# Performance work log

Hardware: AMD Instinct MI355X
Metric: run time of the kernel (lower is better)

## Reference

```python
import jax, jax.numpy as jnp
import numpy as np

D_MODEL = 1024
D_HIDDEN = 4096
NUM_BANKS = 16
NUM_SELECTED = 2


def setup_inputs() -> dict:
    key = jax.random.key(0)
    ks = jax.random.split(key, 7)
    s = 0.02
    return {
        "tensor": jax.random.normal(ks[0], (4, 1024, D_MODEL), dtype=jnp.float32),
        "Wr": jax.random.normal(ks[1], (D_MODEL, NUM_BANKS), dtype=jnp.float32) * s,
        "br": jnp.zeros((NUM_BANKS,), dtype=jnp.float32),
        "W1": jax.random.normal(ks[2], (NUM_BANKS, D_MODEL, D_HIDDEN), dtype=jnp.float32) * s,
        "b1": jnp.zeros((NUM_BANKS, D_HIDDEN), dtype=jnp.float32),
        "W2": jax.random.normal(ks[3], (NUM_BANKS, D_HIDDEN, D_MODEL), dtype=jnp.float32) * s,
        "b2": jnp.zeros((NUM_BANKS, D_MODEL), dtype=jnp.float32),
    }


def reference(tensor, Wr, br, W1, b1, W2, b2):
    # Router: softmax over banks, keep top-k probabilities (BankSelector)
    logits = jnp.einsum("bsd,de->bse", tensor, Wr) + br          # [B,S,E]
    probs = jax.nn.softmax(logits, axis=-1)
    topv, topi = jax.lax.top_k(probs, NUM_SELECTED)              # [B,S,K]
    # Dense gate [B,S,E]: selected banks carry their router probability,
    # all other banks are zeroed (equivalent to sparse dispatch/combine).
    gate = jnp.sum(jax.nn.one_hot(topi, NUM_BANKS, dtype=tensor.dtype)
                   * topv[..., None], axis=-2)                    # [B,S,E]
    # Banked expert FFN (BankedLinear x2 with ReLU between)
    h = jax.nn.relu(jnp.einsum("bsd,edh->bseh", tensor, W1) + b1)  # [B,S,E,Dh]
    y = jnp.einsum("bseh,ehm->bsem", h, W2) + b2                   # [B,S,E,Dm]
    # Weighted combine across selected banks
    out = jnp.einsum("bse,bsem->bsm", gate, y)                     # [B,S,Dm]
    return out
```

## Files before the change

kernel.cpp:

```cpp
#include <hip/hip_runtime.h>
#include <stdint.h>

#define D_MODEL   1024
#define D_HIDDEN  4096
#define NBANKS    16
#define NTOK      4096

#define BM 128
#define BN 128
#define BK 32
#define TBUF (BM * BK)
#define KS2 4

typedef __attribute__((ext_vector_type(8))) short bf16x8;
typedef __attribute__((ext_vector_type(4))) float f32x4;
typedef __attribute__((ext_vector_type(4))) unsigned int u32x4;
typedef __attribute__((ext_vector_type(2))) unsigned int u32x2;

__device__ __forceinline__ unsigned short f2bf(float f) {
  unsigned u = __builtin_bit_cast(unsigned, f);
  u += 0x7FFFu + ((u >> 16) & 1u);
  return (unsigned short)(u >> 16);
}

__device__ __forceinline__ unsigned cvtpk(float lo, float hi) {
  unsigned r;
  asm("v_cvt_pk_bf16_f32 %0, %1, %2" : "=v"(r) : "v"(lo), "v"(hi));
  return r;
}

__device__ __forceinline__ int sidx(int r, int k) {
  return (r << 5) + ((((k >> 3) ^ ((r >> 2) & 3)) << 3) | (k & 7));
}

__global__ __launch_bounds__(256) void zero_out_k(float4* __restrict__ out4,
                                                  int* __restrict__ counts) {
  size_t i = (size_t)blockIdx.x * 256 + threadIdx.x;
  out4[i] = make_float4(0.f, 0.f, 0.f, 0.f);
  if (blockIdx.x == 0 && threadIdx.x < NBANKS) counts[threadIdx.x] = 0;
}

__global__ __launch_bounds__(256) void cvtx_k(const float* __restrict__ X,
                                              unsigned short* __restrict__ Xb) {
  const size_t i = ((size_t)blockIdx.x * 256 + threadIdx.x) * 8;
  const float4 a = *(const float4*)(X + i);
  const float4 b = *(const float4*)(X + i + 4);
  u32x4 v;
  v[0] = cvtpk(a.x, a.y); v[1] = cvtpk(a.z, a.w);
  v[2] = cvtpk(b.x, b.y); v[3] = cvtpk(b.z, b.w);
  *(u32x4*)(Xb + i) = v;
}

__global__ __launch_bounds__(64) void router_k(const float* __restrict__ x,
                                               const float* __restrict__ Wr,
                                               const float* __restrict__ br,
                                               int* __restrict__ topIdx,
                                               float* __restrict__ topGate) {
  const int t = blockIdx.x;
  const int l = threadIdx.x;
  const float* xr = x + (size_t)t * D_MODEL;

  float acc[NBANKS];
#pragma unroll
  for (int e = 0; e < NBANKS; ++e) acc[e] = 0.f;

  for (int d = l; d < D_MODEL; d += 64) {
    const float xv = xr[d];
    const float* wrow = Wr + (size_t)d * NBANKS;
#pragma unroll
    for (int e = 0; e < NBANKS; ++e) acc[e] += xv * wrow[e];
  }
#pragma unroll
  for (int e = 0; e < NBANKS; ++e) {
#pragma unroll
    for (int m = 1; m < 64; m <<= 1) acc[e] += __shfl_xor(acc[e], m, 64);
  }
#pragma unroll
  for (int e = 0; e < NBANKS; ++e) acc[e] += br[e];

  if (l == 0) {
    float mx = acc[0];
#pragma unroll
    for (int e = 1; e < NBANKS; ++e) mx = fmaxf(mx, acc[e]);
    float p[NBANKS];
    float s = 0.f;
#pragma unroll
    for (int e = 0; e < NBANKS; ++e) { p[e] = expf(acc[e] - mx); s += p[e]; }
    int i0 = 0; float v0 = p[0];
#pragma unroll
    for (int e = 1; e < NBANKS; ++e) if (p[e] > v0) { v0 = p[e]; i0 = e; }
    int i1 = -1; float v1 = -1.f;
#pragma unroll
    for (int e = 0; e < NBANKS; ++e) if (e != i0 && p[e] > v1) { v1 = p[e]; i1 = e; }
    const float inv = 1.f / s;
    topIdx[2 * t]     = i0;
    topIdx[2 * t + 1] = i1;
    topGate[2 * t]     = v0 * inv;
    topGate[2 * t + 1] = v1 * inv;
  }
}

__global__ __launch_bounds__(256) void build_lists_k(const int* __restrict__ topIdx,
                                                     const float* __restrict__ topGate,
                                                     int* __restrict__ counts,
                                                     int* __restrict__ rowlist,
                                                     float* __restrict__ gatelist) {
  const int t = blockIdx.x * 256 + threadIdx.x;
  if (t >= NTOK) return;
#pragma unroll
  for (int k = 0; k < 2; ++k) {
    const int e = topIdx[2 * t + k];
    const int p = atomicAdd(&counts[e], 1);
    rowlist[e * NTOK + p]  = t;
    gatelist[e * NTOK + p] = topGate[2 * t + k];
  }
}

__global__ void scan_k(const int* __restrict__ counts, int* __restrict__ bankOff) {
  if (threadIdx.x == 0) {
    int s = 0;
#pragma unroll
    for (int e = 0; e < NBANKS; ++e) { bankOff[e] = s; s += counts[e]; }
    bankOff[NBANKS] = s;
  }
}

__global__ __launch_bounds__(256, 2) void gemm1_k(const unsigned short* __restrict__ Xb,
                                                  const float* __restrict__ W1,
                                                  const float* __restrict__ b1,
                                                  const int* __restrict__ counts,
                                                  const int* __restrict__ bankOff,
                                                  const int* __restrict__ rowlist,
                                                  unsigned short* __restrict__ H) {
  const int e   = blockIdx.z;
  const int cnt = counts[e];
  const int m0  = blockIdx.y * BM;
  if (m0 >= cnt) return;
  const int n0  = blockIdx.x * BN;

  const int tid  = threadIdx.x;
  const int lane = tid & 63;
  const int w    = tid >> 6;
  const int wm   = (w >> 1) * 64;
  const int wn   = (w & 1) * 64;

  __shared__ unsigned short Xs[2 * TBUF];
  __shared__ unsigned short Ws[2 * TBUF];

  const int arow = tid >> 1;
  const int ak   = (tid & 1) * 16;
  const int gi   = min(m0 + arow, cnt - 1);
  const int tok  = rowlist[e * NTOK + gi];
  const unsigned short* Asrc = Xb + (size_t)tok * D_MODEL + ak;
  const int xo0 = sidx(arow, ak);
  const int xo1 = sidx(arow, ak + 8);

  const int n4 = 4 * (tid & 31);
  const int k4 = 4 * (tid >> 5);
  const float* Bsrc = W1 + (size_t)e * D_MODEL * D_HIDDEN + (size_t)k4 * D_HIDDEN + n0 + n4;
  int wo[4];
#pragma unroll
  for (int i = 0; i < 4; ++i) wo[i] = sidx(n4 + i, k4);

  const int fr = lane & 15;
  const int fc = (lane >> 4) * 8;
  int aoff[4], boff[4];
#pragma unroll
  for (int i = 0; i < 4; ++i) {
    aoff[i] = sidx(wm + i * 16 + fr, fc);
    boff[i] = sidx(wn + i * 16 + fr, fc);
  }

  bf16x8 ra0, ra1;
  float rbf[4][4];

  f32x4 acc[4][4];
#pragma unroll
  for (int i = 0; i < 4; ++i)
#pragma unroll
    for (int j = 0; j < 4; ++j)
#pragma unroll
      for (int r = 0; r < 4; ++r) acc[i][j][r] = 0.f;

  unsigned short* xc = &Xs[0];       unsigned short* wc = &Ws[0];
  unsigned short* xn = &Xs[TBUF];    unsigned short* wn_ = &Ws[TBUF];

  auto LOAD = [&](int t) {
    const unsigned short* ap = Asrc + t * BK;
    ra0 = *(const bf16x8*)(ap);
    ra1 = *(const bf16x8*)(ap + 8);
    const float* bp = Bsrc + (size_t)t * BK * D_HIDDEN;
#pragma unroll
    for (int kk = 0; kk < 4; ++kk)
      *(float4*)&rbf[kk][0] = *(const float4*)(bp + (size_t)kk * D_HIDDEN);
  };

  auto WRITE = [&](unsigned short* xs, unsigned short* ws) {
    *(bf16x8*)(xs + xo0) = ra0;
    *(bf16x8*)(xs + xo1) = ra1;
#pragma unroll
    for (int i = 0; i < 4; ++i) {
      u32x2 v;
      v[0] = cvtpk(rbf[0][i], rbf[1][i]);
      v[1] = cvtpk(rbf[2][i], rbf[3][i]);
      *(u32x2*)(ws + wo[i]) = v;
    }
  };

  auto COMPUTE = [&](const unsigned short* xs, const unsigned short* ws) {
    bf16x8 af[4], bb[4];
#pragma unroll
    for (int mb = 0; mb < 4; ++mb) af[mb] = *(const bf16x8*)(xs + aoff[mb]);
#pragma unroll
    for (int nb = 0; nb < 4; ++nb) bb[nb] = *(const bf16x8*)(ws + boff[nb]);
#pragma unroll
    for (int mb = 0; mb < 4; ++mb)
#pragma unroll
      for (int nb = 0; nb < 4; ++nb)
        acc[mb][nb] = __builtin_amdgcn_mfma_f32_16x16x32_bf16(af[mb], bb[nb], acc[mb][nb], 0, 0, 0);
  };

  const int NT = D_MODEL / BK;
  LOAD(0);
  WRITE(xc, wc);
  __syncthreads();
#pragma unroll 1
  for (int t = 0; t < NT; ++t) {
    if (t + 1 < NT) LOAD(t + 1);
    __builtin_amdgcn_sched_barrier(0);
    COMPUTE(xc, wc);
    if (t + 1 < NT) WRITE(xn, wn_);
    __syncthreads();
    unsigned short* t0 = xc; xc = xn;  xn  = t0;
    unsigned short* t1 = wc; wc = wn_; wn_ = t1;
  }

  const int hb = bankOff[e] + m0;
  const int rq = (lane >> 4) * 4;
#pragma unroll
  for (int nb = 0; nb < 4; ++nb) {
    const int col = n0 + wn + nb * 16 + fr;
    const float bias = b1[e * D_HIDDEN + col];
#pragma unroll
    for (int mb = 0; mb < 4; ++mb)
#pragma unroll
      for (int r = 0; r < 4; ++r) {
        const int rowT = wm + mb * 16 + rq + r;
        if (m0 + rowT < cnt) {
          float v = acc[mb][nb][r] + bias;
          v = fmaxf(v, 0.f);
          H[(size_t)(hb + rowT) * D_HIDDEN + col] = f2bf(v);
        }
      }
  }
}

__global__ __launch_bounds__(256, 2) void gemm2_k(const unsigned short* __restrict__ H,
                                                  const float* __restrict__ W2,
                                                  const float* __restrict__ b2,
                                                  const int* __restrict__ counts,
                                                  const int* __restrict__ bankOff,
                                                  const int* __restrict__ rowlist,
                                                  const float* __restrict__ gatelist,
                                                  float* __restrict__ out) {
  const int z   = blockIdx.z;
  const int e   = z >> 2;
  const int kc  = z & 3;
  const int cnt = counts[e];
  const int m0  = blockIdx.y * BM;
  if (m0 >= cnt) return;
  const int n0  = blockIdx.x * BN;
  const int kc0 = kc * (D_HIDDEN / KS2);

  const int tid  = threadIdx.x;
  const int lane = tid & 63;
  const int w    = tid >> 6;
  const int wm   = (w >> 1) * 64;
  const int wn   = (w & 1) * 64;

  __shared__ unsigned short Xs[2 * TBUF];
  __shared__ unsigned short Ws[2 * TBUF];

  const int arow = tid >> 1;
  const int ak   = (tid & 1) * 16;
  const int hb   = bankOff[e];
  const int gi   = hb + min(m0 + arow, cnt - 1);
  const unsigned short* Asrc = H + (size_t)gi * D_HIDDEN + kc0 + ak;
  const int xo0 = sidx(arow, ak);
  const int xo1 = sidx(arow, ak + 8);

  const int n4 = 4 * (tid & 31);
  const int k4 = 4 * (tid >> 5);
  const float* Bsrc = W2 + (size_t)e * D_HIDDEN * D_MODEL + (size_t)(kc0 + k4) * D_MODEL + n0 + n4;
  int wo[4];
#pragma unroll
  for (int i = 0; i < 4; ++i) wo[i] = sidx(n4 + i, k4);

  const int fr = lane & 15;
  const int fc = (lane >> 4) * 8;
  int aoff[4], boff[4];
#pragma unroll
  for (int i = 0; i < 4; ++i) {
    aoff[i] = sidx(wm + i * 16 + fr, fc);
    boff[i] = sidx(wn + i * 16 + fr, fc);
  }

  bf16x8 ra0, ra1;
  float rbf[4][4];

  f32x4 acc[4][4];
#pragma unroll
  for (int i = 0; i < 4; ++i)
#pragma unroll
    for (int j = 0; j < 4; ++j)
#pragma unroll
      for (int r = 0; r < 4; ++r) acc[i][j][r] = 0.f;

  unsigned short* xc = &Xs[0];       unsigned short* wc = &Ws[0];
  unsigned short* xn = &Xs[TBUF];    unsigned short* wn_ = &Ws[TBUF];

  auto LOAD = [&](int t) {
    const unsigned short* ap = Asrc + t * BK;
    ra0 = *(const bf16x8*)(ap);
    ra1 = *(const bf16x8*)(ap + 8);
    const float* bp = Bsrc + (size_t)t * BK * D_MODEL;
#pragma unroll
    for (int kk = 0; kk < 4; ++kk)
      *(float4*)&rbf[kk][0] = *(const float4*)(bp + (size_t)kk * D_MODEL);
  };

  auto WRITE = [&](unsigned short* xs, unsigned short* ws) {
    *(bf16x8*)(xs + xo0) = ra0;
    *(bf16x8*)(xs + xo1) = ra1;
#pragma unroll
    for (int i = 0; i < 4; ++i) {
      u32x2 v;
      v[0] = cvtpk(rbf[0][i], rbf[1][i]);
      v[1] = cvtpk(rbf[2][i], rbf[3][i]);
      *(u32x2*)(ws + wo[i]) = v;
    }
  };

  auto COMPUTE = [&](const unsigned short* xs, const unsigned short* ws) {
    bf16x8 af[4], bb[4];
#pragma unroll
    for (int mb = 0; mb < 4; ++mb) af[mb] = *(const bf16x8*)(xs + aoff[mb]);
#pragma unroll
    for (int nb = 0; nb < 4; ++nb) bb[nb] = *(const bf16x8*)(ws + boff[nb]);
#pragma unroll
    for (int mb = 0; mb < 4; ++mb)
#pragma unroll
      for (int nb = 0; nb < 4; ++nb)
        acc[mb][nb] = __builtin_amdgcn_mfma_f32_16x16x32_bf16(af[mb], bb[nb], acc[mb][nb], 0, 0, 0);
  };

  const int NT = (D_HIDDEN / KS2) / BK;
  LOAD(0);
  WRITE(xc, wc);
  __syncthreads();
#pragma unroll 1
  for (int t = 0; t < NT; ++t) {
    if (t + 1 < NT) LOAD(t + 1);
    __builtin_amdgcn_sched_barrier(0);
    COMPUTE(xc, wc);
    if (t + 1 < NT) WRITE(xn, wn_);
    __syncthreads();
    unsigned short* t0 = xc; xc = xn;  xn  = t0;
    unsigned short* t1 = wc; wc = wn_; wn_ = t1;
  }

  const int rq = (lane >> 4) * 4;
  float bias[4];
#pragma unroll
  for (int nb = 0; nb < 4; ++nb)
    bias[nb] = (kc == 0) ? b2[e * D_MODEL + n0 + wn + nb * 16 + fr] : 0.f;

#pragma unroll
  for (int mb = 0; mb < 4; ++mb)
#pragma unroll
    for (int r = 0; r < 4; ++r) {
      const int rowT = wm + mb * 16 + rq + r;
      if (m0 + rowT < cnt) {
        const int si = e * NTOK + m0 + rowT;
        const int tok = rowlist[si];
        const float g = gatelist[si];
        float* orow = out + (size_t)tok * D_MODEL;
#pragma unroll
        for (int nb = 0; nb < 4; ++nb) {
          const int col = n0 + wn + nb * 16 + fr;
          atomicAdd(&orow[col], g * (acc[mb][nb][r] + bias[nb]));
        }
      }
    }
}

extern "C" void kernel_launch(void* const* d_in, const int* in_sizes, int n_in,
                              void* d_out, int out_size, void* d_ws, size_t ws_size,
                              hipStream_t stream) {
  const float* X  = (const float*)d_in[0];
  const float* Wr = (const float*)d_in[1];
  const float* br = (const float*)d_in[2];
  const float* W1 = (const float*)d_in[3];
  const float* b1 = (const float*)d_in[4];
  const float* W2 = (const float*)d_in[5];
  const float* b2 = (const float*)d_in[6];
  float* out = (float*)d_out;

  char* w = (char*)d_ws;
  int*   topIdx   = (int*)(w);
  float* topGate  = (float*)(w + (32 << 10));
  int*   counts   = (int*)(w + (64 << 10));
  int*   bankOff  = (int*)(w + (64 << 10) + 256);
  int*   rowlist  = (int*)(w + (66 << 10));
  float* gatelist = (float*)(w + (66 << 10) + NBANKS * NTOK * 4);
  unsigned short* Xb = (unsigned short*)(w + (1 << 20));
  unsigned short* H  = (unsigned short*)(w + (16 << 20));

  const size_t needed = (size_t)(16 << 20) + (size_t)(NTOK * 2) * D_HIDDEN * 2;
  if (ws_size < needed) return;

  zero_out_k<<<dim3(4096), dim3(256), 0, stream>>>((float4*)out, counts);
  cvtx_k<<<dim3(NTOK * D_MODEL / 8 / 256), dim3(256), 0, stream>>>(X, Xb);
  router_k<<<dim3(NTOK), dim3(64), 0, stream>>>(X, Wr, br, topIdx, topGate);
  build_lists_k<<<dim3(16), dim3(256), 0, stream>>>(topIdx, topGate, counts, rowlist, gatelist);
  scan_k<<<dim3(1), dim3(64), 0, stream>>>(counts, bankOff);
  gemm1_k<<<dim3(D_HIDDEN / BN, NTOK / BM, NBANKS), dim3(256), 0, stream>>>(
      Xb, W1, b1, counts, bankOff, rowlist, H);
  gemm2_k<<<dim3(D_MODEL / BN, NTOK / BM, NBANKS * KS2), dim3(256), 0, stream>>>(
      H, W2, b2, counts, bankOff, rowlist, gatelist, out);
}
```

Measured before the change: 450.1 us.

## Compact grouped-GEMM grid via precomputed tile list and adjust LDS swizzle

```diff
diff --git a/kernel.cpp b/kernel.cpp
--- a/kernel.cpp
+++ b/kernel.cpp
@@ -11,6 +11,7 @@
 #define BK 32
 #define TBUF (BM * BK)
 #define KS2 4
+#define MAXT 512
 
 typedef __attribute__((ext_vector_type(8))) short bf16x8;
 typedef __attribute__((ext_vector_type(4))) float f32x4;
@@ -30,7 +31,7 @@
 }
 
 __device__ __forceinline__ int sidx(int r, int k) {
-  return (r << 5) + ((((k >> 3) ^ ((r >> 2) & 3)) << 3) | (k & 7));
+  return (r << 5) + ((((k >> 3) ^ ((r >> 1) & 3)) << 3) | (k & 7));
 }
 
 __global__ __launch_bounds__(256) void zero_out_k(float4* __restrict__ out4,
@@ -116,12 +117,24 @@
   }
 }
 
-__global__ void scan_k(const int* __restrict__ counts, int* __restrict__ bankOff) {
+__global__ void scan_k(const int* __restrict__ counts, int* __restrict__ bankOff,
+                       int* __restrict__ tileE, int* __restrict__ tileM,
+                       int* __restrict__ nT) {
   if (threadIdx.x == 0) {
     int s = 0;
-#pragma unroll
-    for (int e = 0; e < NBANKS; ++e) { bankOff[e] = s; s += counts[e]; }
+    int t = 0;
+    for (int e = 0; e < NBANKS; ++e) {
+      bankOff[e] = s;
+      const int c = counts[e];
+      s += c;
+      for (int m = 0; m < c; m += BM) {
+        tileE[t] = e;
+        tileM[t] = m;
+        ++t;
+      }
+    }
     bankOff[NBANKS] = s;
+    nT[0] = t;
   }
 }
 
@@ -131,11 +144,15 @@
                                                   const int* __restrict__ counts,
                                                   const int* __restrict__ bankOff,
                                                   const int* __restrict__ rowlist,
+                                                  const int* __restrict__ tileE,
+                                                  const int* __restrict__ tileM,
+                                                  const int* __restrict__ nT,
                                                   unsigned short* __restrict__ H) {
-  const int e   = blockIdx.z;
+  const int tI = blockIdx.y;
+  if (tI >= nT[0]) return;
+  const int e   = tileE[tI];
+  const int m0  = tileM[tI];
   const int cnt = counts[e];
-  const int m0  = blockIdx.y * BM;
-  if (m0 >= cnt) return;
   const int n0  = blockIdx.x * BN;
 
   const int tid  = threadIdx.x;
@@ -262,13 +279,16 @@
                                                   const int* __restrict__ bankOff,
                                                   const int* __restrict__ rowlist,
                                                   const float* __restrict__ gatelist,
+                                                  const int* __restrict__ tileE,
+                                                  const int* __restrict__ tileM,
+                                                  const int* __restrict__ nT,
                                                   float* __restrict__ out) {
-  const int z   = blockIdx.z;
-  const int e   = z >> 2;
-  const int kc  = z & 3;
+  const int tI = blockIdx.y >> 2;
+  const int kc = blockIdx.y & 3;
+  if (tI >= nT[0]) return;
+  const int e   = tileE[tI];
+  const int m0  = tileM[tI];
   const int cnt = counts[e];
-  const int m0  = blockIdx.y * BM;
-  if (m0 >= cnt) return;
   const int n0  = blockIdx.x * BN;
   const int kc0 = kc * (D_HIDDEN / KS2);
 
@@ -413,6 +433,9 @@
   int*   bankOff  = (int*)(w + (64 << 10) + 256);
   int*   rowlist  = (int*)(w + (66 << 10));
   float* gatelist = (float*)(w + (66 << 10) + NBANKS * NTOK * 4);
+  int*   tileE    = (int*)(w + (600 << 10));
+  int*   tileM    = (int*)(w + (604 << 10));
+  int*   nT       = (int*)(w + (608 << 10));
   unsigned short* Xb = (unsigned short*)(w + (1 << 20));
   unsigned short* H  = (unsigned short*)(w + (16 << 20));
 
@@ -423,9 +446,9 @@
   cvtx_k<<<dim3(NTOK * D_MODEL / 8 / 256), dim3(256), 0, stream>>>(X, Xb);
   router_k<<<dim3(NTOK), dim3(64), 0, stream>>>(X, Wr, br, topIdx, topGate);
   build_lists_k<<<dim3(16), dim3(256), 0, stream>>>(topIdx, topGate, counts, rowlist, gatelist);
-  scan_k<<<dim3(1), dim3(64), 0, stream>>>(counts, bankOff);
-  gemm1_k<<<dim3(D_HIDDEN / BN, NTOK / BM, NBANKS), dim3(256), 0, stream>>>(
-      Xb, W1, b1, counts, bankOff, rowlist, H);
-  gemm2_k<<<dim3(D_MODEL / BN, NTOK / BM, NBANKS * KS2), dim3(256), 0, stream>>>(
-      H, W2, b2, counts, bankOff, rowlist, gatelist, out);
-}
+  scan_k<<<dim3(1), dim3(64), 0, stream>>>(counts, bankOff, tileE, tileM, nT);
+  gemm1_k<<<dim3(D_HIDDEN / BN, MAXT), dim3(256), 0, stream>>>(
+      Xb, W1, b1, counts, bankOff, rowlist, tileE, tileM, nT, H);
+  gemm2_k<<<dim3(D_MODEL / BN, MAXT * KS2), dim3(256), 0, stream>>>(
+      H, W2, b2, counts, bankOff, rowlist, gatelist, tileE, tileM, nT, out);
+}
```

Result: slower. 460.9 us (+2.4%).
